# Optimization experiments

Measured on AMD Instinct MI355X. Metric: run time of the kernel, lower is better.

Reference implementation:

```python
import jax, jax.numpy as jnp
import numpy as np

B, T, N, S = 128, 1024, 128, 256
NEG = jnp.float32(-1e30)  # acts as -inf but keeps grads finite


def setup_inputs() -> dict:
    key = jax.random.key(0)
    k1, k2, k3, k4, k5 = jax.random.split(key, 5)
    inputs = jax.random.normal(k1, (B, T, N), dtype=jnp.float32)
    # nn.Parameter inits to zeros; use small noise so transition actually participates
    transition = 0.05 * jax.random.normal(k2, (N, N), dtype=jnp.float32)
    targets = jax.random.randint(k3, (B, S), 0, N)
    input_lengths = jax.random.randint(k4, (B,), T // 2, T + 1).astype(jnp.int32)
    target_lengths = jax.random.randint(k5, (B,), S // 2, S + 1).astype(jnp.int32)
    return {
        "transition": transition,
        "inputs": inputs,
        "targets": targets,
        "input_lengths": input_lengths,
        "target_lengths": target_lengths,
    }


def reference(transition, inputs, targets, input_lengths, target_lengths):
    # ASG loss = FCC (free-running partition) - FAC (forced alignment score),
    # scale_mode='none', reduction='mean'. transition[j, i] = score of label i -> j.
    xs = jnp.moveaxis(inputs, 1, 0)  # (T, B, N)
    ts = jnp.arange(1, T)

    # ---- FCC: alpha[t, b, j] = x[t,b,j] + logsumexp_i(alpha[t-1,b,i] + trans[j,i])
    def fcc_step(alpha, xt):
        x_t, t = xt
        new = x_t + jax.nn.logsumexp(alpha[:, None, :] + transition[None, :, :], axis=-1)
        return jnp.where((t < input_lengths)[:, None], new, alpha), None

    alphaT, _ = jax.lax.scan(fcc_step, xs[0], (xs[1:], ts))
    fcc = jax.nn.logsumexp(alphaT, axis=-1)  # (B,)

    # ---- FAC: beta[t, b, s] over target positions, self/next transitions only
    self_tr = transition[targets, targets]  # (B, S): stay on targets[s]
    prev_lbl = jnp.concatenate([targets[:, :1], targets[:, :-1]], axis=1)
    next_tr = transition[targets, prev_lbl]  # (B, S): targets[s-1] -> targets[s]

    em0 = jnp.take_along_axis(xs[0], targets, axis=1)  # (B, S)
    beta0 = jnp.where(jnp.arange(S)[None, :] == 0, em0, NEG)

    def fac_step(beta, xt):
        x_t, t = xt
        em = jnp.take_along_axis(x_t, targets, axis=1)  # (B, S)
        shifted = jnp.concatenate(
            [jnp.full((B, 1), NEG, dtype=beta.dtype), beta[:, :-1]], axis=1
        )
        new = em + jnp.logaddexp(beta + self_tr, shifted + next_tr)
        return jnp.where((t < input_lengths)[:, None], new, beta), None

    betaT, _ = jax.lax.scan(fac_step, beta0, (xs[1:], ts))
    fac = jnp.take_along_axis(betaT, (target_lengths - 1)[:, None], axis=1)[:, 0]

    return jnp.mean(fcc - fac)
```

## Files before the change

### kernel.cpp

```cpp
#include <hip/hip_runtime.h>
#include <hip/hip_bf16.h>

#define Bb 128
#define Tt 1024
#define Nn 128
#define Ss 256
#define NEGF (-1e30f)
#define D9 9.0f

typedef __attribute__((ext_vector_type(8))) short short8;
typedef __attribute__((ext_vector_type(4))) float f32x4;

__device__ __forceinline__ short bf16b(float f) {
    __hip_bfloat16 h = __float2bfloat16(f);
    return *reinterpret_cast<short*>(&h);
}

#define LDS_BARRIER() asm volatile("s_waitcnt lgkmcnt(0)\n\ts_barrier" ::: "memory")

#define FCC_STEP(t_, k_)                                                       \
    {                                                                          \
        const int t = (t_);                                                    \
        if ((k_) == 0) { \
            float m = fmaxf(fmaxf(wred[0][g], wred[1][g]),                     \
                            fmaxf(wred[2][g], wred[3][g]));                    \
            if (t < len) {                                                     \
                float invm = 1.0f / m;                                         \
                wc[0][0] *= invm; wc[0][1] *= invm;                            \
                wc[0][2] *= invm; wc[0][3] *= invm;                            \
                wc[1][0] *= invm; wc[1][1] *= invm;                            \
                wc[1][2] *= invm; wc[1][3] *= invm;                            \
                c += __logf(m);                                                \
            }                                                                  \
        }                                                                      \
        const short* up = &ut[(t - 1) & 1][g][0] + quad * 8;                   \
        short8 bf0 = *(const short8*)(up);                                     \
        short8 bf1 = *(const short8*)(up + 32);                                \
        short8 bf2 = *(const short8*)(up + 64);                                \
        short8 bf3 = *(const short8*)(up + 96);                                \
        f32x4 a0p = {0.f, 0.f, 0.f, 0.f}, a0q = {0.f, 0.f, 0.f, 0.f};          \
        f32x4 a1p = {0.f, 0.f, 0.f, 0.f}, a1q = {0.f, 0.f, 0.f, 0.f};          \
        a0p = __builtin_amdgcn_mfma_f32_16x16x32_bf16(ea[0][0], bf0, a0p, 0, 0, 0); \
        a1p = __builtin_amdgcn_mfma_f32_16x16x32_bf16(ea[1][0], bf0, a1p, 0, 0, 0); \
        a0q = __builtin_amdgcn_mfma_f32_16x16x32_bf16(ea[0][2], bf2, a0q, 0, 0, 0); \
        a1q = __builtin_amdgcn_mfma_f32_16x16x32_bf16(ea[1][2], bf2, a1q, 0, 0, 0); \
        a0p = __builtin_amdgcn_mfma_f32_16x16x32_bf16(ea[0][1], bf1, a0p, 0, 0, 0); \
        a1p = __builtin_amdgcn_mfma_f32_16x16x32_bf16(ea[1][1], bf1, a1p, 0, 0, 0); \
        a0q = __builtin_amdgcn_mfma_f32_16x16x32_bf16(ea[0][3], bf3, a0q, 0, 0, 0); \
        a1q = __builtin_amdgcn_mfma_f32_16x16x32_bf16(ea[1][3], bf3, a1q, 0, 0, 0); \
        const bool act = (t < len);                                            \
        float un[2][4];                                                        \
        un[0][0] = act ? wc[0][0] * (a0p[0] + a0q[0]) : uprev[0][0];           \
        un[0][1] = act ? wc[0][1] * (a0p[1] + a0q[1]) : uprev[0][1];           \
        un[0][2] = act ? wc[0][2] * (a0p[2] + a0q[2]) : uprev[0][2];           \
        un[0][3] = act ? wc[0][3] * (a0p[3] + a0q[3]) : uprev[0][3];           \
        un[1][0] = act ? wc[1][0] * (a1p[0] + a1q[0]) : uprev[1][0];           \
        un[1][1] = act ? wc[1][1] * (a1p[1] + a1q[1]) : uprev[1][1];           \
        un[1][2] = act ? wc[1][2] * (a1p[2] + a1q[2]) : uprev[1][2];           \
        un[1][3] = act ? wc[1][3] * (a1p[3] + a1q[3]) : uprev[1][3];           \
        uprev[0][0] = un[0][0]; uprev[0][1] = un[0][1];                        \
        uprev[0][2] = un[0][2]; uprev[0][3] = un[0][3];                        \
        uprev[1][0] = un[1][0]; uprev[1][1] = un[1][1];                        \
        uprev[1][2] = un[1][2]; uprev[1][3] = un[1][3];                        \
        {                                                                      \
            short4 s4;                                                         \
            s4.x = bf16b(un[0][0]); s4.y = bf16b(un[0][1]);                    \
            s4.z = bf16b(un[0][2]); s4.w = bf16b(un[0][3]);                    \
            *reinterpret_cast<short4*>(&ut[t & 1][g][j0_]) = s4;               \
            s4.x = bf16b(un[1][0]); s4.y = bf16b(un[1][1]);                    \
            s4.z = bf16b(un[1][2]); s4.w = bf16b(un[1][3]);                    \
            *reinterpret_cast<short4*>(&ut[t & 1][g][j0_ + 16]) = s4;          \
        }                                                                      \
               \
        const int sl = ((k_) + 1) & 3;                                         \
        wc[0][0] = __expf(xs[sl][0].x - D9);                                   \
        wc[0][1] = __expf(xs[sl][0].y - D9);                                   \
        wc[0][2] = __expf(xs[sl][0].z - D9);                                   \
        wc[0][3] = __expf(xs[sl][0].w - D9);                                   \
        wc[1][0] = __expf(xs[sl][1].x - D9);                                   \
        wc[1][1] = __expf(xs[sl][1].y - D9);                                   \
        wc[1][2] = __expf(xs[sl][1].z - D9);                                   \
        wc[1][3] = __expf(xs[sl][1].w - D9);                                   \
             \
              \
        {                                                                      \
            int kk = t + 5; if (kk > Tt - 1) kk = Tt - 1;                      \
            xs[sl][0] = *(const float4*)(xb + (size_t)kk * Nn + j0_);          \
            xs[sl][1] = *(const float4*)(xb + (size_t)kk * Nn + j0_ + 16);     \
        }                                                                      \
        if ((k_) == 7) {                                   \
            float mm = un[0][0];                                               \
            mm = fmaxf(mm, un[0][1]); mm = fmaxf(mm, un[0][2]);                \
            mm = fmaxf(mm, un[0][3]); mm = fmaxf(mm, un[1][0]);                \
            mm = fmaxf(mm, un[1][1]); mm = fmaxf(mm, un[1][2]);                \
            mm = fmaxf(mm, un[1][3]);                                          \
            mm = fmaxf(mm, __shfl_xor(mm, 16));                                \
            mm = fmaxf(mm, __shfl_xor(mm, 32));                                \
            if (lane < 16) wred[q][lane] = mm;                                 \
        }                                                                      \
        LDS_BARRIER();                                                         \
    }

#define FAC_STEP(t_, k_)                                                       \
    {                                                                          \
        const int t = (t_);                                                    \
        const int d = ((k_) + 7) & 7;                                          \
        float e0 = em[d][0], e1 = em[d][1], e2 = em[d][2], e3 = em[d][3];      \
        int tn = t + 8; if (tn > Tt - 1) tn = Tt - 1;                          \
        const float* xrow = xb + (size_t)tn * Nn;                              \
        em[d][0] = xrow[tgi[0]]; em[d][1] = xrow[tgi[1]];                      \
        em[d][2] = xrow[tgi[2]]; em[d][3] = xrow[tgi[3]];                      \
        float bup = __shfl_up(bt[3], 1);                                       \
        float prev0 = (lane == 0) ? NEGF : bup;                                \
        float nb[4];                                                           \
        {                                                                      \
            float aa = bt[0] + st[0], bb = prev0 + ntr[0];                     \
            float hi = fmaxf(aa, bb), lo = fminf(aa, bb);                      \
            nb[0] = e0 + hi + __logf(1.0f + __expf(lo - hi));                  \
        }                                                                      \
        {                                                                      \
            float aa = bt[1] + st[1], bb = bt[0] + ntr[1];                     \
            float hi = fmaxf(aa, bb), lo = fminf(aa, bb);                      \
            nb[1] = e1 + hi + __logf(1.0f + __expf(lo - hi));                  \
        }                                                                      \
        {                                                                      \
            float aa = bt[2] + st[2], bb = bt[1] + ntr[2];                     \
            float hi = fmaxf(aa, bb), lo = fminf(aa, bb);                      \
            nb[2] = e2 + hi + __logf(1.0f + __expf(lo - hi));                  \
        }                                                                      \
        {                                                                      \
            float aa = bt[3] + st[3], bb = bt[2] + ntr[3];                     \
            float hi = fmaxf(aa, bb), lo = fminf(aa, bb);                      \
            nb[3] = e3 + hi + __logf(1.0f + __expf(lo - hi));                  \
        }                                                                      \
        if (t < len) {                                                         \
            bt[0] = nb[0]; bt[1] = nb[1]; bt[2] = nb[2]; bt[3] = nb[3];        \
        }                                                                      \
    }

__global__ __launch_bounds__(256) void asg_main(
    const float* __restrict__ trans, const float* __restrict__ x,
    const int* __restrict__ targets, const int* __restrict__ ilen,
    const int* __restrict__ tlen,
    float* __restrict__ fcc_out, float* __restrict__ fac_out)
{
    __shared__ __align__(16) short ut[2][16][136];
    __shared__ float wred[4][16];

    const int tid  = threadIdx.x;
    const int q    = tid >> 6;
    const int lane = tid & 63;
    const int g    = lane & 15;
    const int quad = lane >> 4;

    if (blockIdx.x < 8) {
        const int b   = (blockIdx.x << 4) + g;
        const int len = ilen[b];
        const float* xb = x + (size_t)b * Tt * Nn;

        short8 ea[2][4];
        #pragma unroll
        for (int mt = 0; mt < 2; ++mt) {
            const float* tr = trans + (size_t)(32 * q + 16 * mt + g) * Nn + quad * 8;
            #pragma unroll
            for (int kc = 0; kc < 4; ++kc) {
                short8 v;
                #pragma unroll
                for (int jj = 0; jj < 8; ++jj)
                    v[jj] = bf16b(__expf(tr[kc * 32 + jj]));
                ea[mt][kc] = v;
            }
        }

        const int j0_ = 32 * q + 4 * quad;

        float uprev[2][4];
        #pragma unroll
        for (int mt = 0; mt < 2; ++mt) {
            const int j0 = j0_ + 16 * mt;
            float4 xv = *(const float4*)(xb + j0);
            uprev[mt][0] = __expf(xv.x); uprev[mt][1] = __expf(xv.y);
            uprev[mt][2] = __expf(xv.z); uprev[mt][3] = __expf(xv.w);
            short4 s4;
            s4.x = bf16b(uprev[mt][0]); s4.y = bf16b(uprev[mt][1]);
            s4.z = bf16b(uprev[mt][2]); s4.w = bf16b(uprev[mt][3]);
            *reinterpret_cast<short4*>(&ut[0][g][j0]) = s4;
        }

        float wc[2][4];
        float4 xs[4][2];
        #pragma unroll
        for (int mt = 0; mt < 2; ++mt) {
            const int j0 = j0_ + 16 * mt;
            float4 xv = *(const float4*)(xb + Nn + j0);
            wc[mt][0] = __expf(xv.x - D9); wc[mt][1] = __expf(xv.y - D9);
            wc[mt][2] = __expf(xv.z - D9); wc[mt][3] = __expf(xv.w - D9);
            #pragma unroll
            for (int k = 2; k <= 5; ++k)
                xs[k & 3][mt] = *(const float4*)(xb + (size_t)k * Nn + j0);
        }
        float c = 0.0f;
        __syncthreads();

        #pragma unroll
        for (int k = 1; k < 8; ++k) FCC_STEP(k, k)
        for (int tb = 8; tb < Tt; tb += 8) {
            #pragma unroll
            for (int k = 0; k < 8; ++k) FCC_STEP(tb + k, k)
        }

        c += D9 * (float)(len - 1);

        float s = 0.f;
        #pragma unroll
        for (int mt = 0; mt < 2; ++mt)
            #pragma unroll
            for (int r = 0; r < 4; ++r) s += uprev[mt][r];
        s += __shfl_xor(s, 16);
        s += __shfl_xor(s, 32);
        if (lane < 16) wred[q][lane] = s;
        __syncthreads();
        if (tid < 16) {
            float tot = wred[0][tid] + wred[1][tid] + wred[2][tid] + wred[3][tid];
            fcc_out[(blockIdx.x << 4) + tid] = c + __logf(tot);
        }
    } else {
        const int b   = ((blockIdx.x - 8) << 2) + q;
        const int len = ilen[b];
        const int tl  = tlen[b];
        const float* xb = x + (size_t)b * Tt * Nn;

        int   tgi[4];
        float st[4], ntr[4], bt[4];
        #pragma unroll
        for (int r = 0; r < 4; ++r) {
            const int s = (lane << 2) + r;
            const int tgv = targets[b * Ss + s];
            const int pg  = (s == 0) ? tgv : targets[b * Ss + s - 1];
            tgi[r] = tgv;
            st[r]  = trans[tgv * Nn + tgv];
            ntr[r] = trans[tgv * Nn + pg];
            bt[r]  = (s == 0) ? xb[tgv] : NEGF;
        }
        float em[8][4];
        #pragma unroll
        for (int k = 1; k <= 8; ++k) {
            int tt = k; if (tt > Tt - 1) tt = Tt - 1;
            const float* xrow = xb + (size_t)tt * Nn;
            em[(k - 1) & 7][0] = xrow[tgi[0]];
            em[(k - 1) & 7][1] = xrow[tgi[1]];
            em[(k - 1) & 7][2] = xrow[tgi[2]];
            em[(k - 1) & 7][3] = xrow[tgi[3]];
        }

        #pragma unroll
        for (int k = 1; k < 8; ++k) FAC_STEP(k, k)
        for (int tb = 8; tb < Tt; tb += 8) {
            #pragma unroll
            for (int k = 0; k < 8; ++k) FAC_STEP(tb + k, k)
        }

        #pragma unroll
        for (int r = 0; r < 4; ++r)
            if ((lane << 2) + r == tl - 1) fac_out[b] = bt[r];
    }
}

__global__ __launch_bounds__(128) void reduce_kernel(const float* __restrict__ fcc,
                                                     const float* __restrict__ fac,
                                                     float* __restrict__ out) {
    __shared__ float r2[2];
    int tid = threadIdx.x;
    float v = fcc[tid] - fac[tid];
    #pragma unroll
    for (int o = 32; o > 0; o >>= 1) v += __shfl_xor(v, o);
    if ((tid & 63) == 0) r2[tid >> 6] = v;
    __syncthreads();
    if (tid == 0) out[0] = (r2[0] + r2[1]) * (1.0f / Bb);
}

extern "C" void kernel_launch(void* const* d_in, const int* in_sizes, int n_in,
                              void* d_out, int out_size, void* d_ws, size_t ws_size,
                              hipStream_t stream) {
    const float* trans   = (const float*)d_in[0];
    const float* x       = (const float*)d_in[1];
    const int*   targets = (const int*)d_in[2];
    const int*   ilen    = (const int*)d_in[3];
    const int*   tlen    = (const int*)d_in[4];
    float* out = (float*)d_out;

    float* fcc = (float*)d_ws;
    float* fac = fcc + Bb;

    asg_main<<<8 + Bb / 4, 256, 0, stream>>>(trans, x, targets, ilen, tlen, fcc, fac);
    reduce_kernel<<<1, 128, 0, stream>>>(fcc, fac, out);
}
```

Measured before the change: 393.3 us.

## Restructure FCC recursion to one wave per 16 batches, keeping state in registers

```diff
diff --git a/kernel.cpp b/kernel.cpp
--- a/kernel.cpp
+++ b/kernel.cpp
@@ -16,89 +16,73 @@
     return *reinterpret_cast<short*>(&h);
 }
 
-#define LDS_BARRIER() asm volatile("s_waitcnt lgkmcnt(0)\n\ts_barrier" ::: "memory")
+#define WV(v) (PRE ? (v) : __expf((v) - D9))
 
 #define FCC_STEP(t_, k_)                                                       \
     {                                                                          \
         const int t = (t_);                                                    \
-        if ((k_) == 0) { \
-            float m = fmaxf(fmaxf(wred[0][g], wred[1][g]),                     \
-                            fmaxf(wred[2][g], wred[3][g]));                    \
-            if (t < len) {                                                     \
-                float invm = 1.0f / m;                                         \
-                wc[0][0] *= invm; wc[0][1] *= invm;                            \
-                wc[0][2] *= invm; wc[0][3] *= invm;                            \
-                wc[1][0] *= invm; wc[1][1] *= invm;                            \
-                wc[1][2] *= invm; wc[1][3] *= invm;                            \
-                c += __logf(m);                                                \
+        const int sl = (k_) & 3;        \
+        float p[8][4];                                                         \
+        _Pragma("unroll")                                                      \
+        for (int mt = 0; mt < 8; ++mt) {                                       \
+            p[mt][0] = WV(xs[sl][mt][0]) * acc[mt][0];                         \
+            p[mt][1] = WV(xs[sl][mt][1]) * acc[mt][1];                         \
+            p[mt][2] = WV(xs[sl][mt][2]) * acc[mt][2];                         \
+            p[mt][3] = WV(xs[sl][mt][3]) * acc[mt][3];                         \
+        }                                                                      \
+        if ((k_) == 0) {  \
+            float invm = 1.0f / rm;                                            \
+            c += __logf(rm);                                                   \
+            _Pragma("unroll")                                                  \
+            for (int mt = 0; mt < 8; ++mt) {                                   \
+                p[mt][0] *= invm; p[mt][1] *= invm;                            \
+                p[mt][2] *= invm; p[mt][3] *= invm;                            \
             }                                                                  \
         }                                                                      \
-        const short* up = &ut[(t - 1) & 1][g][0] + quad * 8;                   \
-        short8 bf0 = *(const short8*)(up);                                     \
-        short8 bf1 = *(const short8*)(up + 32);                                \
-        short8 bf2 = *(const short8*)(up + 64);                                \
-        short8 bf3 = *(const short8*)(up + 96);                                \
-        f32x4 a0p = {0.f, 0.f, 0.f, 0.f}, a0q = {0.f, 0.f, 0.f, 0.f};          \
-        f32x4 a1p = {0.f, 0.f, 0.f, 0.f}, a1q = {0.f, 0.f, 0.f, 0.f};          \
-        a0p = __builtin_amdgcn_mfma_f32_16x16x32_bf16(ea[0][0], bf0, a0p, 0, 0, 0); \
-        a1p = __builtin_amdgcn_mfma_f32_16x16x32_bf16(ea[1][0], bf0, a1p, 0, 0, 0); \
-        a0q = __builtin_amdgcn_mfma_f32_16x16x32_bf16(ea[0][2], bf2, a0q, 0, 0, 0); \
-        a1q = __builtin_amdgcn_mfma_f32_16x16x32_bf16(ea[1][2], bf2, a1q, 0, 0, 0); \
-        a0p = __builtin_amdgcn_mfma_f32_16x16x32_bf16(ea[0][1], bf1, a0p, 0, 0, 0); \
-        a1p = __builtin_amdgcn_mfma_f32_16x16x32_bf16(ea[1][1], bf1, a1p, 0, 0, 0); \
-        a0q = __builtin_amdgcn_mfma_f32_16x16x32_bf16(ea[0][3], bf3, a0q, 0, 0, 0); \
-        a1q = __builtin_amdgcn_mfma_f32_16x16x32_bf16(ea[1][3], bf3, a1q, 0, 0, 0); \
-        const bool act = (t < len);                                            \
-        float un[2][4];                                                        \
-        un[0][0] = act ? wc[0][0] * (a0p[0] + a0q[0]) : uprev[0][0];           \
-        un[0][1] = act ? wc[0][1] * (a0p[1] + a0q[1]) : uprev[0][1];           \
-        un[0][2] = act ? wc[0][2] * (a0p[2] + a0q[2]) : uprev[0][2];           \
-        un[0][3] = act ? wc[0][3] * (a0p[3] + a0q[3]) : uprev[0][3];           \
-        un[1][0] = act ? wc[1][0] * (a1p[0] + a1q[0]) : uprev[1][0];           \
-        un[1][1] = act ? wc[1][1] * (a1p[1] + a1q[1]) : uprev[1][1];           \
-        un[1][2] = act ? wc[1][2] * (a1p[2] + a1q[2]) : uprev[1][2];           \
-        un[1][3] = act ? wc[1][3] * (a1p[3] + a1q[3]) : uprev[1][3];           \
-        uprev[0][0] = un[0][0]; uprev[0][1] = un[0][1];                        \
-        uprev[0][2] = un[0][2]; uprev[0][3] = un[0][3];                        \
-        uprev[1][0] = un[1][0]; uprev[1][1] = un[1][1];                        \
-        uprev[1][2] = un[1][2]; uprev[1][3] = un[1][3];                        \
-        {                                                                      \
-            short4 s4;                                                         \
-            s4.x = bf16b(un[0][0]); s4.y = bf16b(un[0][1]);                    \
-            s4.z = bf16b(un[0][2]); s4.w = bf16b(un[0][3]);                    \
-            *reinterpret_cast<short4*>(&ut[t & 1][g][j0_]) = s4;               \
-            s4.x = bf16b(un[1][0]); s4.y = bf16b(un[1][1]);                    \
-            s4.z = bf16b(un[1][2]); s4.w = bf16b(un[1][3]);                    \
-            *reinterpret_cast<short4*>(&ut[t & 1][g][j0_ + 16]) = s4;          \
-        }                                                                      \
-               \
-        const int sl = ((k_) + 1) & 3;                                         \
-        wc[0][0] = __expf(xs[sl][0].x - D9);                                   \
-        wc[0][1] = __expf(xs[sl][0].y - D9);                                   \
-        wc[0][2] = __expf(xs[sl][0].z - D9);                                   \
-        wc[0][3] = __expf(xs[sl][0].w - D9);                                   \
-        wc[1][0] = __expf(xs[sl][1].x - D9);                                   \
-        wc[1][1] = __expf(xs[sl][1].y - D9);                                   \
-        wc[1][2] = __expf(xs[sl][1].z - D9);                                   \
-        wc[1][3] = __expf(xs[sl][1].w - D9);                                   \
-             \
-              \
-        {                                                                      \
-            int kk = t + 5; if (kk > Tt - 1) kk = Tt - 1;                      \
-            xs[sl][0] = *(const float4*)(xb + (size_t)kk * Nn + j0_);          \
-            xs[sl][1] = *(const float4*)(xb + (size_t)kk * Nn + j0_ + 16);     \
-        }                                                                      \
-        if ((k_) == 7) {                                   \
-            float mm = un[0][0];                                               \
-            mm = fmaxf(mm, un[0][1]); mm = fmaxf(mm, un[0][2]);                \
-            mm = fmaxf(mm, un[0][3]); mm = fmaxf(mm, un[1][0]);                \
-            mm = fmaxf(mm, un[1][1]); mm = fmaxf(mm, un[1][2]);                \
-            mm = fmaxf(mm, un[1][3]);                                          \
+        if (t == len - 1) {    \
+            float s = 0.f;                                                     \
+            _Pragma("unroll")                                                  \
+            for (int mt = 0; mt < 8; ++mt)                                     \
+                s += (p[mt][0] + p[mt][1]) + (p[mt][2] + p[mt][3]);            \
+            s += __shfl_xor(s, 16);                                            \
+            s += __shfl_xor(s, 32);                                            \
+            sfin = s; cfin = c;                                                \
+        }                                                                      \
+        _Pragma("unroll")                                                      \
+        for (int kc = 0; kc < 4; ++kc) {                                       \
+            short8 v;                                                          \
+            v[0] = bf16b(p[2 * kc][0]);     v[1] = bf16b(p[2 * kc][1]);        \
+            v[2] = bf16b(p[2 * kc][2]);     v[3] = bf16b(p[2 * kc][3]);        \
+            v[4] = bf16b(p[2 * kc + 1][0]); v[5] = bf16b(p[2 * kc + 1][1]);    \
+            v[6] = bf16b(p[2 * kc + 1][2]); v[7] = bf16b(p[2 * kc + 1][3]);    \
+            fr[kc] = v;                                                        \
+        }                                                                      \
+        if ((k_) == 7) { \
+            float mm = fmaxf(fmaxf(p[0][0], p[0][1]), fmaxf(p[0][2], p[0][3]));\
+            _Pragma("unroll")                                                  \
+            for (int mt = 1; mt < 8; ++mt)                                     \
+                mm = fmaxf(mm, fmaxf(fmaxf(p[mt][0], p[mt][1]),                \
+                                     fmaxf(p[mt][2], p[mt][3])));              \
             mm = fmaxf(mm, __shfl_xor(mm, 16));                                \
             mm = fmaxf(mm, __shfl_xor(mm, 32));                                \
-            if (lane < 16) wred[q][lane] = mm;                                 \
-        }                                                                      \
-        LDS_BARRIER();                                                         \
+            rm = mm;                                                           \
+        }                                                                      \
+        {       \
+            int kk = t + 4; if (kk > Tt - 1) kk = Tt - 1;                      \
+            const f32x4* src = (const f32x4*)(wb + (size_t)kk * Nn);           \
+            _Pragma("unroll")                                                  \
+            for (int mt = 0; mt < 8; ++mt) xs[sl][mt] = src[mt];               \
+        }                                                                      \
+        const f32x4 zz = {0.f, 0.f, 0.f, 0.f};                                 \
+        _Pragma("unroll")                                                      \
+        for (int mt = 0; mt < 8; ++mt)                                         \
+            acc[mt] = __builtin_amdgcn_mfma_f32_16x16x32_bf16(ea[mt][0], fr[0], zz, 0, 0, 0); \
+        _Pragma("unroll")                                                      \
+        for (int kc = 1; kc < 4; ++kc) {                                       \
+            _Pragma("unroll")                                                  \
+            for (int mt = 0; mt < 8; ++mt)                                     \
+                acc[mt] = __builtin_amdgcn_mfma_f32_16x16x32_bf16(ea[mt][kc], fr[kc], acc[mt], 0, 0, 0); \
+        }                                                                      \
     }
 
 #define FAC_STEP(t_, k_)                                                       \
@@ -138,69 +122,94 @@
         }                                                                      \
     }
 
-__global__ __launch_bounds__(256) void asg_main(
+__global__ __launch_bounds__(256) void exp_w_kernel(const float* __restrict__ x,
+                                                    float* __restrict__ w) {
+    const size_t total  = (size_t)Bb * Tt * Nn;
+    const size_t stride = (size_t)gridDim.x * 256 * 4;
+    for (size_t i = ((size_t)blockIdx.x * 256 + threadIdx.x) * 4; i < total; i += stride) {
+        f32x4 v = *(const f32x4*)(x + i);
+        f32x4 o;
+        o[0] = __expf(v[0] - D9); o[1] = __expf(v[1] - D9);
+        o[2] = __expf(v[2] - D9); o[3] = __expf(v[3] - D9);
+        *(f32x4*)(w + i) = o;
+    }
+}
+
+template <bool PRE>
+__global__ __launch_bounds__(256, 1) void asg_main(
     const float* __restrict__ trans, const float* __restrict__ x,
+    const float* __restrict__ W,
     const int* __restrict__ targets, const int* __restrict__ ilen,
     const int* __restrict__ tlen,
     float* __restrict__ fcc_out, float* __restrict__ fac_out)
 {
-    __shared__ __align__(16) short ut[2][16][136];
-    __shared__ float wred[4][16];
-
     const int tid  = threadIdx.x;
     const int q    = tid >> 6;
     const int lane = tid & 63;
-    const int g    = lane & 15;
-    const int quad = lane >> 4;
-
-    if (blockIdx.x < 8) {
-        const int b   = (blockIdx.x << 4) + g;
+
+    if (blockIdx.x < 2) {
+        const int h  = lane >> 4;
+        const int cc = lane & 15;
+        const int wv = (blockIdx.x << 2) + q;
+        const int b  = (wv << 4) + cc;
         const int len = ilen[b];
-        const float* xb = x + (size_t)b * Tt * Nn;
-
-        short8 ea[2][4];
-        #pragma unroll
-        for (int mt = 0; mt < 2; ++mt) {
-            const float* tr = trans + (size_t)(32 * q + 16 * mt + g) * Nn + quad * 8;
+        const float* wb = (PRE ? W : x) + (size_t)b * Tt * Nn + 32 * h;
+
+        short8 ea[8][4];
+        #pragma unroll
+        for (int mt = 0; mt < 8; ++mt) {
+            const int srow = 32 * (cc >> 2) + 4 * mt + (cc & 3);
+            const float* tr = trans + (size_t)srow * Nn + 32 * h;
             #pragma unroll
             for (int kc = 0; kc < 4; ++kc) {
                 short8 v;
                 #pragma unroll
                 for (int jj = 0; jj < 8; ++jj)
-                    v[jj] = bf16b(__expf(tr[kc * 32 + jj]));
+                    v[jj] = bf16b(__expf(tr[8 * kc + jj]));
                 ea[mt][kc] = v;
             }
         }
 
-        const int j0_ = 32 * q + 4 * quad;
-
-        float uprev[2][4];
-        #pragma unroll
-        for (int mt = 0; mt < 2; ++mt) {
-            const int j0 = j0_ + 16 * mt;
-            float4 xv = *(const float4*)(xb + j0);
-            uprev[mt][0] = __expf(xv.x); uprev[mt][1] = __expf(xv.y);
-            uprev[mt][2] = __expf(xv.z); uprev[mt][3] = __expf(xv.w);
-            short4 s4;
-            s4.x = bf16b(uprev[mt][0]); s4.y = bf16b(uprev[mt][1]);
-            s4.z = bf16b(uprev[mt][2]); s4.w = bf16b(uprev[mt][3]);
-            *reinterpret_cast<short4*>(&ut[0][g][j0]) = s4;
-        }
-
-        float wc[2][4];
-        float4 xs[4][2];
-        #pragma unroll
-        for (int mt = 0; mt < 2; ++mt) {
-            const int j0 = j0_ + 16 * mt;
-            float4 xv = *(const float4*)(xb + Nn + j0);
-            wc[mt][0] = __expf(xv.x - D9); wc[mt][1] = __expf(xv.y - D9);
-            wc[mt][2] = __expf(xv.z - D9); wc[mt][3] = __expf(xv.w - D9);
-            #pragma unroll
-            for (int k = 2; k <= 5; ++k)
-                xs[k & 3][mt] = *(const float4*)(xb + (size_t)k * Nn + j0);
-        }
-        float c = 0.0f;
-        __syncthreads();
+        f32x4 acc[8];
+        f32x4 xs[4][8];
+        short8 fr[4];
+        float c = 0.f, rm = 1.0f, sfin = 1.0f, cfin = 0.f;
+
+        {
+            const f32x4* r0 = (const f32x4*)(wb);
+            float p[8][4];
+            #pragma unroll
+            for (int mt = 0; mt < 8; ++mt) {
+                f32x4 v = r0[mt];
+                p[mt][0] = WV(v[0]); p[mt][1] = WV(v[1]);
+                p[mt][2] = WV(v[2]); p[mt][3] = WV(v[3]);
+            }
+            #pragma unroll
+            for (int kc = 0; kc < 4; ++kc) {
+                short8 v;
+                v[0] = bf16b(p[2*kc][0]);   v[1] = bf16b(p[2*kc][1]);
+                v[2] = bf16b(p[2*kc][2]);   v[3] = bf16b(p[2*kc][3]);
+                v[4] = bf16b(p[2*kc+1][0]); v[5] = bf16b(p[2*kc+1][1]);
+                v[6] = bf16b(p[2*kc+1][2]); v[7] = bf16b(p[2*kc+1][3]);
+                fr[kc] = v;
+            }
+            const f32x4 zz = {0.f, 0.f, 0.f, 0.f};
+            #pragma unroll
+            for (int mt = 0; mt < 8; ++mt)
+                acc[mt] = __builtin_amdgcn_mfma_f32_16x16x32_bf16(ea[mt][0], fr[0], zz, 0, 0, 0);
+            #pragma unroll
+            for (int kc = 1; kc < 4; ++kc) {
+                #pragma unroll
+                for (int mt = 0; mt < 8; ++mt)
+                    acc[mt] = __builtin_amdgcn_mfma_f32_16x16x32_bf16(ea[mt][kc], fr[kc], acc[mt], 0, 0, 0);
+            }
+        }
+        #pragma unroll
+        for (int k = 1; k <= 4; ++k) {
+            const f32x4* rr = (const f32x4*)(wb + (size_t)k * Nn);
+            #pragma unroll
+            for (int mt = 0; mt < 8; ++mt) xs[k & 3][mt] = rr[mt];
+        }
 
         #pragma unroll
         for (int k = 1; k < 8; ++k) FCC_STEP(k, k)
@@ -209,23 +218,9 @@
             for (int k = 0; k < 8; ++k) FCC_STEP(tb + k, k)
         }
 
-        c += D9 * (float)(len - 1);
-
-        float s = 0.f;
-        #pragma unroll
-        for (int mt = 0; mt < 2; ++mt)
-            #pragma unroll
-            for (int r = 0; r < 4; ++r) s += uprev[mt][r];
-        s += __shfl_xor(s, 16);
-        s += __shfl_xor(s, 32);
-        if (lane < 16) wred[q][lane] = s;
-        __syncthreads();
-        if (tid < 16) {
-            float tot = wred[0][tid] + wred[1][tid] + wred[2][tid] + wred[3][tid];
-            fcc_out[(blockIdx.x << 4) + tid] = c + __logf(tot);
-        }
+        if (h == 0) fcc_out[b] = cfin + D9 * (float)len + __logf(sfin);
     } else {
-        const int b   = ((blockIdx.x - 8) << 2) + q;
+        const int b   = ((blockIdx.x - 2) << 2) + q;
         const int len = ilen[b];
         const int tl  = tlen[b];
         const float* xb = x + (size_t)b * Tt * Nn;
@@ -291,7 +286,16 @@
 
     float* fcc = (float*)d_ws;
     float* fac = fcc + Bb;
-
-    asg_main<<<8 + Bb / 4, 256, 0, stream>>>(trans, x, targets, ilen, tlen, fcc, fac);
+    float* W   = (float*)((char*)d_ws + 2048);
+
+    const size_t wbytes = (size_t)Bb * Tt * Nn * sizeof(float);
+    const bool pre = ws_size >= wbytes + 2048;
+
+    if (pre) {
+        exp_w_kernel<<<2048, 256, 0, stream>>>(x, W);
+        asg_main<true><<<2 + Bb / 4, 256, 0, stream>>>(trans, x, W, targets, ilen, tlen, fcc, fac);
+    } else {
+        asg_main<false><<<2 + Bb / 4, 256, 0, stream>>>(trans, x, x, targets, ilen, tlen, fcc, fac);
+    }
     reduce_kernel<<<1, 128, 0, stream>>>(fcc, fac, out);
 }
```

Result: slower. 1.052 ms (+167.6%).

## Precompute exp emissions in a separate kernel with a recurrence-friendly layout

Applied to the files above, without the earlier changes.

```diff
diff --git a/kernel.cpp b/kernel.cpp
--- a/kernel.cpp
+++ b/kernel.cpp
@@ -16,22 +16,30 @@
     return *reinterpret_cast<short*>(&h);
 }
 
+__device__ __forceinline__ unsigned int cvt_pk_bf16(float lo, float hi) {
+    unsigned int r;
+    asm("v_cvt_pk_bf16_f32 %0, %1, %2" : "=v"(r) : "v"(lo), "v"(hi));
+    return r;
+}
+
 #define LDS_BARRIER() asm volatile("s_waitcnt lgkmcnt(0)\n\ts_barrier" ::: "memory")
 
 #define FCC_STEP(t_, k_)                                                       \
     {                                                                          \
         const int t = (t_);                                                    \
-        if ((k_) == 0) { \
-            float m = fmaxf(fmaxf(wred[0][g], wred[1][g]),                     \
-                            fmaxf(wred[2][g], wred[3][g]));                    \
-            if (t < len) {                                                     \
-                float invm = 1.0f / m;                                         \
-                wc[0][0] *= invm; wc[0][1] *= invm;                            \
-                wc[0][2] *= invm; wc[0][3] *= invm;                            \
-                wc[1][0] *= invm; wc[1][1] *= invm;                            \
-                wc[1][2] *= invm; wc[1][3] *= invm;                            \
-                c += __logf(m);                                                \
-            }                                                                  \
+        const int sl = (k_) & 3;                   \
+        f32x4 w0 = xs[sl][0], w1 = xs[sl][1];                                  \
+        if (!PRE) {                                                            \
+            w0[0] = __expf(w0[0] - D9); w0[1] = __expf(w0[1] - D9);            \
+            w0[2] = __expf(w0[2] - D9); w0[3] = __expf(w0[3] - D9);            \
+            w1[0] = __expf(w1[0] - D9); w1[1] = __expf(w1[1] - D9);            \
+            w1[2] = __expf(w1[2] - D9); w1[3] = __expf(w1[3] - D9);            \
+        }                                                                      \
+        {     \
+            int tn = t + 4; if (tn > Tt - 1) tn = Tt - 1;                      \
+            const float* gb = wbase + (size_t)tn * TSTR;                       \
+            xs[sl][0] = *(const f32x4*)(gb);                                   \
+            xs[sl][1] = *(const f32x4*)(gb + MSTR);                            \
         }                                                                      \
         const short* up = &ut[(t - 1) & 1][g][0] + quad * 8;                   \
         short8 bf0 = *(const short8*)(up);                                     \
@@ -48,52 +56,32 @@
         a1p = __builtin_amdgcn_mfma_f32_16x16x32_bf16(ea[1][1], bf1, a1p, 0, 0, 0); \
         a0q = __builtin_amdgcn_mfma_f32_16x16x32_bf16(ea[0][3], bf3, a0q, 0, 0, 0); \
         a1q = __builtin_amdgcn_mfma_f32_16x16x32_bf16(ea[1][3], bf3, a1q, 0, 0, 0); \
-        const bool act = (t < len);                                            \
-        float un[2][4];                                                        \
-        un[0][0] = act ? wc[0][0] * (a0p[0] + a0q[0]) : uprev[0][0];           \
-        un[0][1] = act ? wc[0][1] * (a0p[1] + a0q[1]) : uprev[0][1];           \
-        un[0][2] = act ? wc[0][2] * (a0p[2] + a0q[2]) : uprev[0][2];           \
-        un[0][3] = act ? wc[0][3] * (a0p[3] + a0q[3]) : uprev[0][3];           \
-        un[1][0] = act ? wc[1][0] * (a1p[0] + a1q[0]) : uprev[1][0];           \
-        un[1][1] = act ? wc[1][1] * (a1p[1] + a1q[1]) : uprev[1][1];           \
-        un[1][2] = act ? wc[1][2] * (a1p[2] + a1q[2]) : uprev[1][2];           \
-        un[1][3] = act ? wc[1][3] * (a1p[3] + a1q[3]) : uprev[1][3];           \
-        uprev[0][0] = un[0][0]; uprev[0][1] = un[0][1];                        \
-        uprev[0][2] = un[0][2]; uprev[0][3] = un[0][3];                        \
-        uprev[1][0] = un[1][0]; uprev[1][1] = un[1][1];                        \
-        uprev[1][2] = un[1][2]; uprev[1][3] = un[1][3];                        \
-        {                                                                      \
-            short4 s4;                                                         \
-            s4.x = bf16b(un[0][0]); s4.y = bf16b(un[0][1]);                    \
-            s4.z = bf16b(un[0][2]); s4.w = bf16b(un[0][3]);                    \
-            *reinterpret_cast<short4*>(&ut[t & 1][g][j0_]) = s4;               \
-            s4.x = bf16b(un[1][0]); s4.y = bf16b(un[1][1]);                    \
-            s4.z = bf16b(un[1][2]); s4.w = bf16b(un[1][3]);                    \
-            *reinterpret_cast<short4*>(&ut[t & 1][g][j0_ + 16]) = s4;          \
-        }                                                                      \
-               \
-        const int sl = ((k_) + 1) & 3;                                         \
-        wc[0][0] = __expf(xs[sl][0].x - D9);                                   \
-        wc[0][1] = __expf(xs[sl][0].y - D9);                                   \
-        wc[0][2] = __expf(xs[sl][0].z - D9);                                   \
-        wc[0][3] = __expf(xs[sl][0].w - D9);                                   \
-        wc[1][0] = __expf(xs[sl][1].x - D9);                                   \
-        wc[1][1] = __expf(xs[sl][1].y - D9);                                   \
-        wc[1][2] = __expf(xs[sl][1].z - D9);                                   \
-        wc[1][3] = __expf(xs[sl][1].w - D9);                                   \
-             \
-              \
-        {                                                                      \
-            int kk = t + 5; if (kk > Tt - 1) kk = Tt - 1;                      \
-            xs[sl][0] = *(const float4*)(xb + (size_t)kk * Nn + j0_);          \
-            xs[sl][1] = *(const float4*)(xb + (size_t)kk * Nn + j0_ + 16);     \
-        }                                                                      \
-        if ((k_) == 7) {                                   \
-            float mm = un[0][0];                                               \
-            mm = fmaxf(mm, un[0][1]); mm = fmaxf(mm, un[0][2]);                \
-            mm = fmaxf(mm, un[0][3]); mm = fmaxf(mm, un[1][0]);                \
-            mm = fmaxf(mm, un[1][1]); mm = fmaxf(mm, un[1][2]);                \
-            mm = fmaxf(mm, un[1][3]);                                          \
+        if ((k_) == 0) { \
+            float m = fmaxf(fmaxf(wred[0][g], wred[1][g]),                     \
+                            fmaxf(wred[2][g], wred[3][g]));                    \
+            float invm = 1.0f / m;                                             \
+            c += __logf(m);                                                    \
+            w0 *= invm; w1 *= invm;                                            \
+        }                                                                      \
+        f32x4 un0 = w0 * (a0p + a0q);                                          \
+        f32x4 un1 = w1 * (a1p + a1q);                                          \
+        if (t == len - 1) {  \
+            float s = (un0[0] + un0[1]) + (un0[2] + un0[3])                    \
+                    + (un1[0] + un1[1]) + (un1[2] + un1[3]);                   \
+            s += __shfl_xor(s, 16);                                            \
+            s += __shfl_xor(s, 32);                                            \
+            sfin = s; cfin = c;                                                \
+        }                                                                      \
+        {                                                                      \
+            uint2 o0, o1;                                                      \
+            o0.x = cvt_pk_bf16(un0[0], un0[1]); o0.y = cvt_pk_bf16(un0[2], un0[3]); \
+            o1.x = cvt_pk_bf16(un1[0], un1[1]); o1.y = cvt_pk_bf16(un1[2], un1[3]); \
+            *reinterpret_cast<uint2*>(&ut[t & 1][g][j0_]) = o0;                \
+            *reinterpret_cast<uint2*>(&ut[t & 1][g][j0_ + 16]) = o1;           \
+        }                                                                      \
+        if ((k_) == 7) { \
+            float mm = fmaxf(fmaxf(un0[0], un0[1]), fmaxf(un0[2], un0[3]));    \
+            mm = fmaxf(mm, fmaxf(fmaxf(un1[0], un1[1]), fmaxf(un1[2], un1[3])));\
             mm = fmaxf(mm, __shfl_xor(mm, 16));                                \
             mm = fmaxf(mm, __shfl_xor(mm, 32));                                \
             if (lane < 16) wred[q][lane] = mm;                                 \
@@ -138,8 +126,30 @@
         }                                                                      \
     }
 
-__global__ __launch_bounds__(256) void asg_main(
+__global__ __launch_bounds__(256) void exp_w_kernel(const float* __restrict__ x,
+                                                    float* __restrict__ w) {
+    const int nf4 = Bb * Tt * Nn / 4;
+    const int stride = gridDim.x * 256;
+    for (int f = blockIdx.x * 256 + threadIdx.x; f < nf4; f += stride) {
+        const int l    = f & 63;
+        const int mt   = (f >> 6) & 1;
+        const int qq   = (f >> 7) & 3;
+        const int wv   = (f >> 9) & 7;
+        const int t    = f >> 12;
+        const int b    = (wv << 4) + (l & 15);
+        const int j    = (qq << 5) + (mt << 4) + ((l >> 4) << 2);
+        f32x4 v = *(const f32x4*)(x + ((size_t)b * Tt + t) * Nn + j);
+        f32x4 r;
+        r[0] = __expf(v[0] - D9); r[1] = __expf(v[1] - D9);
+        r[2] = __expf(v[2] - D9); r[3] = __expf(v[3] - D9);
+        *(f32x4*)(w + 4 * (size_t)f) = r;
+    }
+}
+
+template <bool PRE>
+__global__ __launch_bounds__(256, 1) void asg_main(
     const float* __restrict__ trans, const float* __restrict__ x,
+    const float* __restrict__ Wm,
     const int* __restrict__ targets, const int* __restrict__ ilen,
     const int* __restrict__ tlen,
     float* __restrict__ fcc_out, float* __restrict__ fac_out)
@@ -150,13 +160,20 @@
     const int tid  = threadIdx.x;
     const int q    = tid >> 6;
     const int lane = tid & 63;
-    const int g    = lane & 15;
-    const int quad = lane >> 4;
 
     if (blockIdx.x < 8) {
-        const int b   = (blockIdx.x << 4) + g;
-        const int len = ilen[b];
-        const float* xb = x + (size_t)b * Tt * Nn;
+        const int g    = lane & 15;
+        const int quad = lane >> 4;
+        const int wv   = blockIdx.x;
+        const int b    = (wv << 4) + g;
+        const int len  = ilen[b];
+        const int j0_  = 32 * q + 4 * quad;
+
+        constexpr int TSTR = PRE ? 16384 : Nn;
+        constexpr int MSTR = PRE ? 64 * 4 : 16;
+        const float* wbase = PRE
+            ? (Wm + (size_t)(((wv << 2) + q) << 1) * 256 + (lane << 2))
+            : (x + (size_t)b * (Tt * Nn) + 32 * q + 4 * quad);
 
         short8 ea[2][4];
         #pragma unroll
@@ -172,34 +189,30 @@
             }
         }
 
-        const int j0_ = 32 * q + 4 * quad;
-
-        float uprev[2][4];
-        #pragma unroll
-        for (int mt = 0; mt < 2; ++mt) {
-            const int j0 = j0_ + 16 * mt;
-            float4 xv = *(const float4*)(xb + j0);
-            uprev[mt][0] = __expf(xv.x); uprev[mt][1] = __expf(xv.y);
-            uprev[mt][2] = __expf(xv.z); uprev[mt][3] = __expf(xv.w);
-            short4 s4;
-            s4.x = bf16b(uprev[mt][0]); s4.y = bf16b(uprev[mt][1]);
-            s4.z = bf16b(uprev[mt][2]); s4.w = bf16b(uprev[mt][3]);
-            *reinterpret_cast<short4*>(&ut[0][g][j0]) = s4;
-        }
-
-        float wc[2][4];
-        float4 xs[4][2];
-        #pragma unroll
-        for (int mt = 0; mt < 2; ++mt) {
-            const int j0 = j0_ + 16 * mt;
-            float4 xv = *(const float4*)(xb + Nn + j0);
-            wc[mt][0] = __expf(xv.x - D9); wc[mt][1] = __expf(xv.y - D9);
-            wc[mt][2] = __expf(xv.z - D9); wc[mt][3] = __expf(xv.w - D9);
-            #pragma unroll
-            for (int k = 2; k <= 5; ++k)
-                xs[k & 3][mt] = *(const float4*)(xb + (size_t)k * Nn + j0);
-        }
-        float c = 0.0f;
+        f32x4 xs[4][2];
+        float c = 0.f, sfin = 1.0f, cfin = 0.f;
+
+        {
+            f32x4 v0 = *(const f32x4*)(wbase);
+            f32x4 v1 = *(const f32x4*)(wbase + MSTR);
+            if (!PRE) {
+                v0[0]=__expf(v0[0]-D9); v0[1]=__expf(v0[1]-D9);
+                v0[2]=__expf(v0[2]-D9); v0[3]=__expf(v0[3]-D9);
+                v1[0]=__expf(v1[0]-D9); v1[1]=__expf(v1[1]-D9);
+                v1[2]=__expf(v1[2]-D9); v1[3]=__expf(v1[3]-D9);
+            }
+            uint2 o0, o1;
+            o0.x = cvt_pk_bf16(v0[0], v0[1]); o0.y = cvt_pk_bf16(v0[2], v0[3]);
+            o1.x = cvt_pk_bf16(v1[0], v1[1]); o1.y = cvt_pk_bf16(v1[2], v1[3]);
+            *reinterpret_cast<uint2*>(&ut[0][g][j0_]) = o0;
+            *reinterpret_cast<uint2*>(&ut[0][g][j0_ + 16]) = o1;
+        }
+        #pragma unroll
+        for (int k = 1; k <= 4; ++k) {
+            const float* rr = wbase + (size_t)k * TSTR;
+            xs[k & 3][0] = *(const f32x4*)(rr);
+            xs[k & 3][1] = *(const f32x4*)(rr + MSTR);
+        }
         __syncthreads();
 
         #pragma unroll
@@ -209,20 +222,11 @@
             for (int k = 0; k < 8; ++k) FCC_STEP(tb + k, k)
         }
 
-        c += D9 * (float)(len - 1);
-
-        float s = 0.f;
-        #pragma unroll
-        for (int mt = 0; mt < 2; ++mt)
-            #pragma unroll
-            for (int r = 0; r < 4; ++r) s += uprev[mt][r];
-        s += __shfl_xor(s, 16);
-        s += __shfl_xor(s, 32);
-        if (lane < 16) wred[q][lane] = s;
+        if (lane < 16) wred[q][lane] = sfin;
         __syncthreads();
-        if (tid < 16) {
-            float tot = wred[0][tid] + wred[1][tid] + wred[2][tid] + wred[3][tid];
-            fcc_out[(blockIdx.x << 4) + tid] = c + __logf(tot);
+        if (q == 0 && lane < 16) {
+            float tot = wred[0][lane] + wred[1][lane] + wred[2][lane] + wred[3][lane];
+            fcc_out[(wv << 4) + lane] = cfin + D9 * (float)len + __logf(tot);
         }
     } else {
         const int b   = ((blockIdx.x - 8) << 2) + q;
@@ -291,7 +295,16 @@
 
     float* fcc = (float*)d_ws;
     float* fac = fcc + Bb;
-
-    asg_main<<<8 + Bb / 4, 256, 0, stream>>>(trans, x, targets, ilen, tlen, fcc, fac);
+    float* Wm  = (float*)((char*)d_ws + 2048);
+
+    const size_t wbytes = (size_t)Bb * Tt * Nn * sizeof(float);
+    const bool pre = ws_size >= wbytes + 2048;
+
+    if (pre) {
+        exp_w_kernel<<<2048, 256, 0, stream>>>(x, Wm);
+        asg_main<true><<<40, 256, 0, stream>>>(trans, x, Wm, targets, ilen, tlen, fcc, fac);
+    } else {
+        asg_main<false><<<40, 256, 0, stream>>>(trans, x, x, targets, ilen, tlen, fcc, fac);
+    }
     reduce_kernel<<<1, 128, 0, stream>>>(fcc, fac, out);
 }
```

New measurement: 389.9 us. Within noise of the previous version (-0.9%).
